# Performance work log

Hardware: AMD Instinct MI355X
Metric: run time of the kernel (lower is better)

The kernel has to match this reference:

```python
import jax, jax.numpy as jnp
import numpy as np

BATCH, SEQ, HIDDEN, HEAD, VDIM = 4, 4096, 256, 64, 64
GAMMA = 0.96875
SCALE_BASE = 512.0


def _xpos(x, downscale):
    # x: [B, L, d] ; standard RetNet XPOS (rotary + exponential position scale)
    L, d = x.shape[1], x.shape[2]
    half = d // 2
    pos = jnp.arange(L, dtype=jnp.float32)
    scale_vec = (jnp.arange(0, d, 2, dtype=jnp.float32) + 0.4 * d) / (1.4 * d)  # [d/2]
    scale = scale_vec[None, :] ** (pos[:, None] / SCALE_BASE)                   # [L, d/2]
    inv_freq = 1.0 / (10000.0 ** (jnp.arange(half, dtype=jnp.float32) / half))  # [d/2]
    sinusoid = pos[:, None] * inv_freq[None, :]                                 # [L, d/2]
    sin, cos = jnp.sin(sinusoid), jnp.cos(sinusoid)
    if downscale:
        scale = 1.0 / scale
    sin2 = jnp.repeat(sin * scale, 2, axis=-1)  # duplicate_interleave -> [L, d]
    cos2 = jnp.repeat(cos * scale, 2, axis=-1)
    x1, x2 = x[..., ::2], x[..., 1::2]
    rot = jnp.stack((-x2, x1), axis=-1).reshape(x.shape)  # rotate_every_two
    return x * cos2[None] + rot * sin2[None]


def setup_inputs() -> dict:
    key = jax.random.key(0)
    k1, k2, k3, k4 = jax.random.split(key, 4)
    X = jax.random.normal(k1, (BATCH, SEQ, HIDDEN), dtype=jnp.float32)
    W_Q = jax.random.normal(k2, (HIDDEN, HEAD), dtype=jnp.float32) / HIDDEN
    W_K = jax.random.normal(k3, (HIDDEN, HEAD), dtype=jnp.float32) / HIDDEN
    W_V = jax.random.normal(k4, (HIDDEN, VDIM), dtype=jnp.float32) / HIDDEN
    return {"X": X, "W_Q": W_Q, "W_K": W_K, "W_V": W_V}


def reference(X, W_Q, W_K, W_V):
    Q = _xpos(X @ W_Q, downscale=False)   # [B, L, d]
    K = _xpos(X @ W_K, downscale=True)    # [B, L, d]
    V = X @ W_V                           # [B, L, v]
    L = X.shape[1]
    n = jnp.arange(L)
    diff = n[:, None] - n[None, :]
    # D[n, m] = gamma^(n-m) for n >= m, else 0 (NaN/overflow-safe via clamped exponent)
    D = jnp.where(diff >= 0,
                  GAMMA ** jnp.where(diff >= 0, diff, 0).astype(jnp.float32),
                  0.0)
    scores = jnp.einsum('bnd,bmd->bnm', Q, K) * D[None]  # [B, L, L]
    return scores @ V                                     # [B, L, v]
```

## Files before the change

### kernel.cpp

```cpp
#include <hip/hip_runtime.h>
#include <hip/hip_bf16.h>
#include <math.h>


#define SEQ    4096
#define NB     4
#define HID    256
#define HD     64
#define WT     4

typedef short          bf16x8 __attribute__((ext_vector_type(8)));
typedef float          f32x4  __attribute__((ext_vector_type(4)));
typedef unsigned short u16;
typedef unsigned int   u32;
typedef u16            u16x8  __attribute__((ext_vector_type(8)));
typedef u16            u16x4  __attribute__((ext_vector_type(4)));

__device__ __forceinline__ u16 f2bf(float f) {
    __hip_bfloat16 h = __float2bfloat16(f);
    return __builtin_bit_cast(u16, h);
}

__global__ __launch_bounds__(256)
void prep_kernel(const float* __restrict__ WQ, const float* __restrict__ WK,
                 const float* __restrict__ WV, float* __restrict__ Tbl,
                 u16* __restrict__ Wf)
{
    const int t = threadIdx.x;
    if (blockIdx.x < 512) {
        const int p = blockIdx.x * 256 + t;
        const int n = p >> 5, i = p & 31;
        const float sv = (2.f * (float)i + 25.6f) / 89.6f;
        const float sc = powf(sv, (float)n * (1.f / 512.f));
        const float inv_freq = 1.f / powf(10000.f, (float)i * (1.f / 32.f));
        float sn, cs;
        sincosf((float)n * inv_freq, &sn, &cs);
        float4 o;
        o.x = cs * sc; o.y = sn * sc;
        o.z = cs / sc; o.w = sn / sc;
        reinterpret_cast<float4*>(Tbl)[p] = o;
    } else {
        const int p = (blockIdx.x - 512) * 256 + t;
        const int lane = p & 63;
        const int kc   = (p >> 6) & 7;
        const int ct   = p >> 9;
        const int col  = ct * 16 + (lane & 15);
        const float* Wsrc = (col < 64) ? WQ : (col < 128) ? WK : WV;
        const int c = col & 63;
        u16x8 hv;
#pragma unroll
        for (int j = 0; j < 8; ++j)
            hv[j] = f2bf(Wsrc[(kc * 32 + (lane >> 4) * 8 + j) * HD + c]);
        *reinterpret_cast<u16x8*>(&Wf[(size_t)p * 8]) = hv;
    }
}

#define XLDS 264

__global__ __launch_bounds__(1024, 4)
void proj_kernel(const float* __restrict__ X, const float* __restrict__ Tbl,
                 const u16* __restrict__ Wf,
                 u16* __restrict__ Qb, u16* __restrict__ Kb, u16* __restrict__ Vb)
{
    __shared__ __align__(16) u16 Xhs[64 * XLDS];
    const int t = threadIdx.x;
    const int row0 = blockIdx.x * 64;

    for (int e = t; e < 64 * 64; e += 1024) {
        const int r = e >> 6, k4 = (e & 63) << 2;
        const float4 xv = *reinterpret_cast<const float4*>(&X[(size_t)(row0 + r) * HID + k4]);
        u16x4 hv;
#pragma unroll
        for (int j = 0; j < 4; ++j) hv[j] = f2bf((&xv.x)[j]);
        *reinterpret_cast<u16x4*>(&Xhs[r * XLDS + k4]) = hv;
    }
    __syncthreads();

    const int lane = t & 63;
    const int w    = t >> 6;
    const int rt   = w >> 2;
    const int ch   = w & 3;
    const int frow = rt * 16 + (lane & 15);
    const int fk   = (lane >> 4) * 8;

    f32x4 acc[3];
#pragma unroll
    for (int i = 0; i < 3; ++i) acc[i] = (f32x4)0.f;

#pragma unroll
    for (int kc = 0; kc < 8; ++kc) {
        const bf16x8 ah = *reinterpret_cast<const bf16x8*>(&Xhs[frow * XLDS + kc * 32 + fk]);
#pragma unroll
        for (int ctp = 0; ctp < 3; ++ctp) {
            const int ct = ch * 3 + ctp;
            const size_t fb = (size_t)((ct * 8 + kc) * 64 + lane) * 8;
            const bf16x8 wh = *reinterpret_cast<const bf16x8*>(&Wf[fb]);
            acc[ctp] = __builtin_amdgcn_mfma_f32_16x16x32_bf16(ah, wh, acc[ctp], 0, 0, 0);
        }
    }

    const int sel   = lane & 1;
    const int c16   = lane & 15;
    const int rbase = (lane >> 4) * 4;

#pragma unroll
    for (int ctp = 0; ctp < 3; ++ctp) {
        const int ct = ch * 3 + ctp;
        float xp[4];
#pragma unroll
        for (int reg = 0; reg < 4; ++reg)
            xp[reg] = __shfl_xor(acc[ctp][reg], 1, 64);
#pragma unroll
        for (int rr = 0; rr < 2; ++rr) {
            const int reg = sel * 2 + rr;
            const float xe = sel ? xp[reg] : acc[ctp][reg];
            const float xo = sel ? acc[ctp][reg] : xp[reg];
            const int r = row0 + rt * 16 + rbase + reg;
            if (ct < 8) {
                const bool isK = ct >= 4;
                const int cq0 = (ct & 3) * 16 + (c16 & ~1);
                const int i   = cq0 >> 1;
                const int n   = r & (SEQ - 1);
                const float4 tb = reinterpret_cast<const float4*>(Tbl)[n * 32 + i];
                const float cs = isK ? tb.z : tb.x;
                const float sn = isK ? tb.w : tb.y;
                const float oe = xe * cs - xo * sn;
                const float oo = xo * cs + xe * sn;
                const u32 hw = (u32)f2bf(oe) | ((u32)f2bf(oo) << 16);
                u32* P = reinterpret_cast<u32*>(isK ? Kb : Qb);
                P[(r * HD + cq0) >> 1] = hw;
            } else {
                const int cv0 = (ct - 8) * 16 + (c16 & ~1);
                const u32 w32 = (u32)f2bf(xe) | ((u32)f2bf(xo) << 16);
                reinterpret_cast<u32*>(Vb)[(r * HD + cv0) >> 1] = w32;
            }
        }
    }
}

#define KRS 72
#define SW  72

__global__ __launch_bounds__(1024, 4)
void retention_kernel(const u16* __restrict__ Qb, const u16* __restrict__ Kb,
                      const u16* __restrict__ Vb, float* __restrict__ Out)
{
    __shared__ __align__(16) u16 Khs[2][64 * KRS];
    __shared__ __align__(16) u16 Vts[3][64 * KRS];
    __shared__ __align__(16) u16 Ss [2][64 * SW];

    const int t    = threadIdx.x;
    const int lane = t & 63;
    const int w    = t >> 6;
    const int rb   = w >> 2;
    const int cb   = w & 3;

    const int flat = blockIdx.x + 64 * blockIdx.y;
    const int work = (flat & 7) * 32 + (flat >> 3);
    const int nt   = work & 63;
    const int b    = work >> 6;
    const int n0   = nt * 64;
    const int bbase = b * SEQ;

    const int half = t >> 9;
    const int th   = t & 511;
    const int srow = th >> 3;
    const int scol = (th & 7) * 8;
    const int vch  = ((srow >> 3) ^ (th & 7)) & 7;
    const int vidx = vch * 8 + (srow & 7);

    const int mt0 = (nt >= WT) ? (nt - WT) : 0;

    {
        const int gk = (bbase + mt0 * 64 + srow) * HD + scol;
        if (half == 0) {
            *reinterpret_cast<u16x8*>(&Khs[0][srow * KRS + scol]) =
                *reinterpret_cast<const u16x8*>(&Kb[gk]);
        } else {
            const u16x8 vv = *reinterpret_cast<const u16x8*>(&Vb[gk]);
#pragma unroll
            for (int j = 0; j < 8; ++j)
                Vts[0][(scol + j) * KRS + vidx] = vv[j];
        }
    }

    const int frow = rb * 16 + (lane & 15);
    const int fk   = (lane >> 4) * 8;
    const size_t gq = (size_t)(bbase + n0 + frow) * HD + fk;
    const bf16x8 qb0 = *reinterpret_cast<const bf16x8*>(&Qb[gq]);
    const bf16x8 qb1 = *reinterpret_cast<const bf16x8*>(&Qb[gq + 32]);
    __syncthreads();

    const float log2g = -0.04580368544f;
    const int nlocB = rb * 16 + (lane >> 4) * 4;
    const int mloc  = cb * 16 + (lane & 15);
    float gd[4]; int dd[4];
#pragma unroll
    for (int reg = 0; reg < 4; ++reg) {
        dd[reg] = nlocB + reg - mloc;
        gd[reg] = exp2f((float)dd[reg] * log2g);
    }

    f32x4 accO = (f32x4)0.f;
    const int mrow = cb * 16 + (lane & 15);
    const int c0 = ((lane >> 4)     ^ (mrow >> 3)) & 7;
    const int c1 = (((lane >> 4) + 4) ^ (mrow >> 3)) & 7;

    int curV = 0;
    for (int mt = mt0, i = 0; mt <= nt; ++mt, ++i) {
        const int cur  = i & 1;
        const int m0   = mt * 64;
        const bool pref = (mt < nt);
        const int wV   = (curV == 2) ? 0 : curV + 1;

        u16x8 pk, pv;
        if (pref) {
            const int gk = (bbase + m0 + 64 + srow) * HD + scol;
            if (half == 0) pk = *reinterpret_cast<const u16x8*>(&Kb[gk]);
            else           pv = *reinterpret_cast<const u16x8*>(&Vb[gk]);
        }

        const bf16x8 kb0 = *reinterpret_cast<const bf16x8*>(&Khs[cur][mrow * KRS + fk]);
        const bf16x8 kb1 = *reinterpret_cast<const bf16x8*>(&Khs[cur][mrow * KRS + 32 + fk]);
        f32x4 accS = (f32x4)0.f;
        accS = __builtin_amdgcn_mfma_f32_16x16x32_bf16(qb0, kb0, accS, 0, 0, 0);
        accS = __builtin_amdgcn_mfma_f32_16x16x32_bf16(qb1, kb1, accS, 0, 0, 0);

        const float gs = exp2f((float)(n0 - m0) * log2g);
#pragma unroll
        for (int reg = 0; reg < 4; ++reg) {
            const int d   = (n0 - m0) + dd[reg];
            const float g = (d >= 0) ? gs * gd[reg] : 0.f;
            Ss[cur][(nlocB + reg) * SW + mloc] = f2bf(accS[reg] * g);
        }

        if (pref) {
            if (half == 0) {
                *reinterpret_cast<u16x8*>(&Khs[cur ^ 1][srow * KRS + scol]) = pk;
            } else {
#pragma unroll
                for (int j = 0; j < 8; ++j)
                    Vts[wV][(scol + j) * KRS + vidx] = pv[j];
            }
        }

        __syncthreads();

        const bf16x8 s0 = *reinterpret_cast<const bf16x8*>(&Ss[cur][frow * SW + fk]);
        const bf16x8 s1 = *reinterpret_cast<const bf16x8*>(&Ss[cur][frow * SW + 32 + fk]);
        const bf16x8 v0 = *reinterpret_cast<const bf16x8*>(&Vts[curV][mrow * KRS + c0 * 8]);
        const bf16x8 v1 = *reinterpret_cast<const bf16x8*>(&Vts[curV][mrow * KRS + c1 * 8]);
        accO = __builtin_amdgcn_mfma_f32_16x16x32_bf16(s0, v0, accO, 0, 0, 0);
        accO = __builtin_amdgcn_mfma_f32_16x16x32_bf16(s1, v1, accO, 0, 0, 0);

        curV = wV;
    }

    const int v = cb * 16 + (lane & 15);
#pragma unroll
    for (int reg = 0; reg < 4; ++reg) {
        const int n = n0 + rb * 16 + (lane >> 4) * 4 + reg;
        Out[(size_t)(bbase + n) * HD + v] = accO[reg];
    }
}

extern "C" void kernel_launch(void* const* d_in, const int* in_sizes, int n_in,
                              void* d_out, int out_size, void* d_ws, size_t ws_size,
                              hipStream_t stream)
{
    const float* X  = (const float*)d_in[0];
    const float* WQ = (const float*)d_in[1];
    const float* WK = (const float*)d_in[2];
    const float* WV = (const float*)d_in[3];
    float* Out = (float*)d_out;

    char* ws = (char*)d_ws;
    const size_t SZ = (size_t)NB * SEQ * HD * sizeof(u16);
    u16* Qb = (u16*)(ws);
    u16* Kb = (u16*)(ws + SZ);
    u16* Vb = (u16*)(ws + 2 * SZ);
    float* Tbl = (float*)(ws + 3 * SZ);
    u16* Wf = (u16*)(ws + 4 * SZ);

    prep_kernel<<<dim3(536), 256, 0, stream>>>(WQ, WK, WV, Tbl, Wf);
    proj_kernel<<<dim3(256), 1024, 0, stream>>>(
        X, Tbl, Wf, Qb, Kb, Vb);
    retention_kernel<<<dim3(64, NB), 1024, 0, stream>>>(
        Qb, Kb, Vb, Out);
}
```

Before: 28.46 us.

## Fuse projection and retention kernels via cooperative launch with grid sync

Merges the projection and retention kernels into one cooperative kernel. A grid-wide sync separates the two phases, and a single shared-memory buffer is reused for both. The goal is to remove one kernel launch and the gap between the two kernels. In exchange it adds the cost of a grid barrier and requires all 256 blocks to be resident at once. It also moves the Wf workspace offset.

```diff
diff --git a/kernel.cpp b/kernel.cpp
--- a/kernel.cpp
+++ b/kernel.cpp
@@ -1,4 +1,5 @@
 #include <hip/hip_runtime.h>
+#include <hip/hip_cooperative_groups.h>
 #include <hip/hip_bf16.h>
 #include <math.h>
 
@@ -8,6 +9,8 @@
 #define HID    256
 #define HD     64
 #define WT     4
+
+namespace cg = cooperative_groups;
 
 typedef short          bf16x8 __attribute__((ext_vector_type(8)));
 typedef float          f32x4  __attribute__((ext_vector_type(4)));
@@ -56,211 +59,213 @@
 }
 
 #define XLDS 264
+#define KRS  72
+#define SW   72
+#define TILE (64 * KRS)
 
 __global__ __launch_bounds__(1024, 4)
-void proj_kernel(const float* __restrict__ X, const float* __restrict__ Tbl,
-                 const u16* __restrict__ Wf,
-                 u16* __restrict__ Qb, u16* __restrict__ Kb, u16* __restrict__ Vb)
+void fused_kernel(const float* __restrict__ X, const float* __restrict__ Tbl,
+                  const u16* __restrict__ Wf,
+                  u16* __restrict__ Qb, u16* __restrict__ Kb, u16* __restrict__ Vb,
+                  float* __restrict__ Out)
 {
-    __shared__ __align__(16) u16 Xhs[64 * XLDS];
-    const int t = threadIdx.x;
-    const int row0 = blockIdx.x * 64;
-
-    for (int e = t; e < 64 * 64; e += 1024) {
-        const int r = e >> 6, k4 = (e & 63) << 2;
-        const float4 xv = *reinterpret_cast<const float4*>(&X[(size_t)(row0 + r) * HID + k4]);
-        u16x4 hv;
-#pragma unroll
-        for (int j = 0; j < 4; ++j) hv[j] = f2bf((&xv.x)[j]);
-        *reinterpret_cast<u16x4*>(&Xhs[r * XLDS + k4]) = hv;
-    }
-    __syncthreads();
-
-    const int lane = t & 63;
-    const int w    = t >> 6;
-    const int rt   = w >> 2;
-    const int ch   = w & 3;
-    const int frow = rt * 16 + (lane & 15);
-    const int fk   = (lane >> 4) * 8;
-
-    f32x4 acc[3];
-#pragma unroll
-    for (int i = 0; i < 3; ++i) acc[i] = (f32x4)0.f;
-
-#pragma unroll
-    for (int kc = 0; kc < 8; ++kc) {
-        const bf16x8 ah = *reinterpret_cast<const bf16x8*>(&Xhs[frow * XLDS + kc * 32 + fk]);
-#pragma unroll
-        for (int ctp = 0; ctp < 3; ++ctp) {
-            const int ct = ch * 3 + ctp;
-            const size_t fb = (size_t)((ct * 8 + kc) * 64 + lane) * 8;
-            const bf16x8 wh = *reinterpret_cast<const bf16x8*>(&Wf[fb]);
-            acc[ctp] = __builtin_amdgcn_mfma_f32_16x16x32_bf16(ah, wh, acc[ctp], 0, 0, 0);
-        }
-    }
-
-    const int sel   = lane & 1;
-    const int c16   = lane & 15;
-    const int rbase = (lane >> 4) * 4;
-
-#pragma unroll
-    for (int ctp = 0; ctp < 3; ++ctp) {
-        const int ct = ch * 3 + ctp;
-        float xp[4];
-#pragma unroll
-        for (int reg = 0; reg < 4; ++reg)
-            xp[reg] = __shfl_xor(acc[ctp][reg], 1, 64);
-#pragma unroll
-        for (int rr = 0; rr < 2; ++rr) {
-            const int reg = sel * 2 + rr;
-            const float xe = sel ? xp[reg] : acc[ctp][reg];
-            const float xo = sel ? acc[ctp][reg] : xp[reg];
-            const int r = row0 + rt * 16 + rbase + reg;
-            if (ct < 8) {
-                const bool isK = ct >= 4;
-                const int cq0 = (ct & 3) * 16 + (c16 & ~1);
-                const int i   = cq0 >> 1;
-                const int n   = r & (SEQ - 1);
-                const float4 tb = reinterpret_cast<const float4*>(Tbl)[n * 32 + i];
-                const float cs = isK ? tb.z : tb.x;
-                const float sn = isK ? tb.w : tb.y;
-                const float oe = xe * cs - xo * sn;
-                const float oo = xo * cs + xe * sn;
-                const u32 hw = (u32)f2bf(oe) | ((u32)f2bf(oo) << 16);
-                u32* P = reinterpret_cast<u32*>(isK ? Kb : Qb);
-                P[(r * HD + cq0) >> 1] = hw;
-            } else {
-                const int cv0 = (ct - 8) * 16 + (c16 & ~1);
-                const u32 w32 = (u32)f2bf(xe) | ((u32)f2bf(xo) << 16);
-                reinterpret_cast<u32*>(Vb)[(r * HD + cv0) >> 1] = w32;
-            }
-        }
-    }
-}
-
-#define KRS 72
-#define SW  72
-
-__global__ __launch_bounds__(1024, 4)
-void retention_kernel(const u16* __restrict__ Qb, const u16* __restrict__ Kb,
-                      const u16* __restrict__ Vb, float* __restrict__ Out)
-{
-    __shared__ __align__(16) u16 Khs[2][64 * KRS];
-    __shared__ __align__(16) u16 Vts[3][64 * KRS];
-    __shared__ __align__(16) u16 Ss [2][64 * SW];
+    __shared__ __align__(16) u16 SMEM[7 * TILE];
 
     const int t    = threadIdx.x;
     const int lane = t & 63;
     const int w    = t >> 6;
-    const int rb   = w >> 2;
-    const int cb   = w & 3;
-
-    const int flat = blockIdx.x + 64 * blockIdx.y;
-    const int work = (flat & 7) * 32 + (flat >> 3);
-    const int nt   = work & 63;
-    const int b    = work >> 6;
-    const int n0   = nt * 64;
-    const int bbase = b * SEQ;
-
-    const int half = t >> 9;
-    const int th   = t & 511;
-    const int srow = th >> 3;
-    const int scol = (th & 7) * 8;
-    const int vch  = ((srow >> 3) ^ (th & 7)) & 7;
-    const int vidx = vch * 8 + (srow & 7);
-
-    const int mt0 = (nt >= WT) ? (nt - WT) : 0;
 
     {
-        const int gk = (bbase + mt0 * 64 + srow) * HD + scol;
-        if (half == 0) {
-            *reinterpret_cast<u16x8*>(&Khs[0][srow * KRS + scol]) =
-                *reinterpret_cast<const u16x8*>(&Kb[gk]);
-        } else {
-            const u16x8 vv = *reinterpret_cast<const u16x8*>(&Vb[gk]);
-#pragma unroll
-            for (int j = 0; j < 8; ++j)
-                Vts[0][(scol + j) * KRS + vidx] = vv[j];
+        u16* Xhs = SMEM;
+        const int row0 = blockIdx.x * 64;
+
+        for (int e = t; e < 64 * 64; e += 1024) {
+            const int r = e >> 6, k4 = (e & 63) << 2;
+            const float4 xv = *reinterpret_cast<const float4*>(&X[(size_t)(row0 + r) * HID + k4]);
+            u16x4 hv;
+#pragma unroll
+            for (int j = 0; j < 4; ++j) hv[j] = f2bf((&xv.x)[j]);
+            *reinterpret_cast<u16x4*>(&Xhs[r * XLDS + k4]) = hv;
+        }
+        __syncthreads();
+
+        const int rt   = w >> 2;
+        const int ch   = w & 3;
+        const int frow = rt * 16 + (lane & 15);
+        const int fk   = (lane >> 4) * 8;
+
+        f32x4 acc[3];
+#pragma unroll
+        for (int i = 0; i < 3; ++i) acc[i] = (f32x4)0.f;
+
+#pragma unroll
+        for (int kc = 0; kc < 8; ++kc) {
+            const bf16x8 ah = *reinterpret_cast<const bf16x8*>(&Xhs[frow * XLDS + kc * 32 + fk]);
+#pragma unroll
+            for (int ctp = 0; ctp < 3; ++ctp) {
+                const int ct = ch * 3 + ctp;
+                const size_t fb = (size_t)((ct * 8 + kc) * 64 + lane) * 8;
+                const bf16x8 wh = *reinterpret_cast<const bf16x8*>(&Wf[fb]);
+                acc[ctp] = __builtin_amdgcn_mfma_f32_16x16x32_bf16(ah, wh, acc[ctp], 0, 0, 0);
+            }
+        }
+
+        const int sel   = lane & 1;
+        const int c16   = lane & 15;
+        const int rbase = (lane >> 4) * 4;
+
+#pragma unroll
+        for (int ctp = 0; ctp < 3; ++ctp) {
+            const int ct = ch * 3 + ctp;
+            float xp[4];
+#pragma unroll
+            for (int reg = 0; reg < 4; ++reg)
+                xp[reg] = __shfl_xor(acc[ctp][reg], 1, 64);
+#pragma unroll
+            for (int rr = 0; rr < 2; ++rr) {
+                const int reg = sel * 2 + rr;
+                const float xe = sel ? xp[reg] : acc[ctp][reg];
+                const float xo = sel ? acc[ctp][reg] : xp[reg];
+                const int r = row0 + rt * 16 + rbase + reg;
+                if (ct < 8) {
+                    const bool isK = ct >= 4;
+                    const int cq0 = (ct & 3) * 16 + (c16 & ~1);
+                    const int i   = cq0 >> 1;
+                    const int n   = r & (SEQ - 1);
+                    const float4 tb = reinterpret_cast<const float4*>(Tbl)[n * 32 + i];
+                    const float cs = isK ? tb.z : tb.x;
+                    const float sn = isK ? tb.w : tb.y;
+                    const float oe = xe * cs - xo * sn;
+                    const float oo = xo * cs + xe * sn;
+                    const u32 hw = (u32)f2bf(oe) | ((u32)f2bf(oo) << 16);
+                    u32* P = reinterpret_cast<u32*>(isK ? Kb : Qb);
+                    P[(r * HD + cq0) >> 1] = hw;
+                } else {
+                    const int cv0 = (ct - 8) * 16 + (c16 & ~1);
+                    const u32 w32 = (u32)f2bf(xe) | ((u32)f2bf(xo) << 16);
+                    reinterpret_cast<u32*>(Vb)[(r * HD + cv0) >> 1] = w32;
+                }
+            }
         }
     }
 
-    const int frow = rb * 16 + (lane & 15);
-    const int fk   = (lane >> 4) * 8;
-    const size_t gq = (size_t)(bbase + n0 + frow) * HD + fk;
-    const bf16x8 qb0 = *reinterpret_cast<const bf16x8*>(&Qb[gq]);
-    const bf16x8 qb1 = *reinterpret_cast<const bf16x8*>(&Qb[gq + 32]);
-    __syncthreads();
-
-    const float log2g = -0.04580368544f;
-    const int nlocB = rb * 16 + (lane >> 4) * 4;
-    const int mloc  = cb * 16 + (lane & 15);
-    float gd[4]; int dd[4];
-#pragma unroll
-    for (int reg = 0; reg < 4; ++reg) {
-        dd[reg] = nlocB + reg - mloc;
-        gd[reg] = exp2f((float)dd[reg] * log2g);
-    }
-
-    f32x4 accO = (f32x4)0.f;
-    const int mrow = cb * 16 + (lane & 15);
-    const int c0 = ((lane >> 4)     ^ (mrow >> 3)) & 7;
-    const int c1 = (((lane >> 4) + 4) ^ (mrow >> 3)) & 7;
-
-    int curV = 0;
-    for (int mt = mt0, i = 0; mt <= nt; ++mt, ++i) {
-        const int cur  = i & 1;
-        const int m0   = mt * 64;
-        const bool pref = (mt < nt);
-        const int wV   = (curV == 2) ? 0 : curV + 1;
-
-        u16x8 pk, pv;
-        if (pref) {
-            const int gk = (bbase + m0 + 64 + srow) * HD + scol;
-            if (half == 0) pk = *reinterpret_cast<const u16x8*>(&Kb[gk]);
-            else           pv = *reinterpret_cast<const u16x8*>(&Vb[gk]);
-        }
-
-        const bf16x8 kb0 = *reinterpret_cast<const bf16x8*>(&Khs[cur][mrow * KRS + fk]);
-        const bf16x8 kb1 = *reinterpret_cast<const bf16x8*>(&Khs[cur][mrow * KRS + 32 + fk]);
-        f32x4 accS = (f32x4)0.f;
-        accS = __builtin_amdgcn_mfma_f32_16x16x32_bf16(qb0, kb0, accS, 0, 0, 0);
-        accS = __builtin_amdgcn_mfma_f32_16x16x32_bf16(qb1, kb1, accS, 0, 0, 0);
-
-        const float gs = exp2f((float)(n0 - m0) * log2g);
+    cg::this_grid().sync();
+
+    {
+        u16* const KhsB = SMEM;
+        u16* const VtsB = SMEM + 2 * TILE;
+        u16* const SsB  = SMEM + 5 * TILE;
+
+        const int rb   = w >> 2;
+        const int cb   = w & 3;
+
+        const int flat = blockIdx.x;
+        const int work = (flat & 7) * 32 + (flat >> 3);
+        const int nt   = work & 63;
+        const int b    = work >> 6;
+        const int n0   = nt * 64;
+        const int bbase = b * SEQ;
+
+        const int half = t >> 9;
+        const int th   = t & 511;
+        const int srow = th >> 3;
+        const int scol = (th & 7) * 8;
+        const int vch  = ((srow >> 3) ^ (th & 7)) & 7;
+        const int vidx = vch * 8 + (srow & 7);
+
+        const int mt0 = (nt >= WT) ? (nt - WT) : 0;
+
+        {
+            const int gk = (bbase + mt0 * 64 + srow) * HD + scol;
+            if (half == 0) {
+                *reinterpret_cast<u16x8*>(&KhsB[srow * KRS + scol]) =
+                    *reinterpret_cast<const u16x8*>(&Kb[gk]);
+            } else {
+                const u16x8 vv = *reinterpret_cast<const u16x8*>(&Vb[gk]);
+#pragma unroll
+                for (int j = 0; j < 8; ++j)
+                    VtsB[(scol + j) * KRS + vidx] = vv[j];
+            }
+        }
+
+        const int frow = rb * 16 + (lane & 15);
+        const int fk   = (lane >> 4) * 8;
+        const size_t gq = (size_t)(bbase + n0 + frow) * HD + fk;
+        const bf16x8 qb0 = *reinterpret_cast<const bf16x8*>(&Qb[gq]);
+        const bf16x8 qb1 = *reinterpret_cast<const bf16x8*>(&Qb[gq + 32]);
+        __syncthreads();
+
+        const float log2g = -0.04580368544f;
+        const int nlocB = rb * 16 + (lane >> 4) * 4;
+        const int mloc  = cb * 16 + (lane & 15);
+        float gd[4]; int dd[4];
 #pragma unroll
         for (int reg = 0; reg < 4; ++reg) {
-            const int d   = (n0 - m0) + dd[reg];
-            const float g = (d >= 0) ? gs * gd[reg] : 0.f;
-            Ss[cur][(nlocB + reg) * SW + mloc] = f2bf(accS[reg] * g);
-        }
-
-        if (pref) {
-            if (half == 0) {
-                *reinterpret_cast<u16x8*>(&Khs[cur ^ 1][srow * KRS + scol]) = pk;
-            } else {
-#pragma unroll
-                for (int j = 0; j < 8; ++j)
-                    Vts[wV][(scol + j) * KRS + vidx] = pv[j];
-            }
-        }
-
-        __syncthreads();
-
-        const bf16x8 s0 = *reinterpret_cast<const bf16x8*>(&Ss[cur][frow * SW + fk]);
-        const bf16x8 s1 = *reinterpret_cast<const bf16x8*>(&Ss[cur][frow * SW + 32 + fk]);
-        const bf16x8 v0 = *reinterpret_cast<const bf16x8*>(&Vts[curV][mrow * KRS + c0 * 8]);
-        const bf16x8 v1 = *reinterpret_cast<const bf16x8*>(&Vts[curV][mrow * KRS + c1 * 8]);
-        accO = __builtin_amdgcn_mfma_f32_16x16x32_bf16(s0, v0, accO, 0, 0, 0);
-        accO = __builtin_amdgcn_mfma_f32_16x16x32_bf16(s1, v1, accO, 0, 0, 0);
-
-        curV = wV;
-    }
-
-    const int v = cb * 16 + (lane & 15);
-#pragma unroll
-    for (int reg = 0; reg < 4; ++reg) {
-        const int n = n0 + rb * 16 + (lane >> 4) * 4 + reg;
-        Out[(size_t)(bbase + n) * HD + v] = accO[reg];
+            dd[reg] = nlocB + reg - mloc;
+            gd[reg] = exp2f((float)dd[reg] * log2g);
+        }
+
+        f32x4 accO = (f32x4)0.f;
+        const int mrow = cb * 16 + (lane & 15);
+        const int c0 = ((lane >> 4)     ^ (mrow >> 3)) & 7;
+        const int c1 = (((lane >> 4) + 4) ^ (mrow >> 3)) & 7;
+
+        int curV = 0;
+        for (int mt = mt0, i = 0; mt <= nt; ++mt, ++i) {
+            const int cur  = i & 1;
+            const int m0   = mt * 64;
+            const bool pref = (mt < nt);
+            const int wV   = (curV == 2) ? 0 : curV + 1;
+
+            u16x8 pk, pv;
+            if (pref) {
+                const int gk = (bbase + m0 + 64 + srow) * HD + scol;
+                if (half == 0) pk = *reinterpret_cast<const u16x8*>(&Kb[gk]);
+                else           pv = *reinterpret_cast<const u16x8*>(&Vb[gk]);
+            }
+
+            const bf16x8 kb0 = *reinterpret_cast<const bf16x8*>(&KhsB[cur * TILE + mrow * KRS + fk]);
+            const bf16x8 kb1 = *reinterpret_cast<const bf16x8*>(&KhsB[cur * TILE + mrow * KRS + 32 + fk]);
+            f32x4 accS = (f32x4)0.f;
+            accS = __builtin_amdgcn_mfma_f32_16x16x32_bf16(qb0, kb0, accS, 0, 0, 0);
+            accS = __builtin_amdgcn_mfma_f32_16x16x32_bf16(qb1, kb1, accS, 0, 0, 0);
+
+            const float gs = exp2f((float)(n0 - m0) * log2g);
+#pragma unroll
+            for (int reg = 0; reg < 4; ++reg) {
+                const int d   = (n0 - m0) + dd[reg];
+                const float g = (d >= 0) ? gs * gd[reg] : 0.f;
+                SsB[cur * TILE + (nlocB + reg) * SW + mloc] = f2bf(accS[reg] * g);
+            }
+
+            if (pref) {
+                if (half == 0) {
+                    *reinterpret_cast<u16x8*>(&KhsB[(cur ^ 1) * TILE + srow * KRS + scol]) = pk;
+                } else {
+#pragma unroll
+                    for (int j = 0; j < 8; ++j)
+                        VtsB[wV * TILE + (scol + j) * KRS + vidx] = pv[j];
+                }
+            }
+
+            __syncthreads();
+
+            const bf16x8 s0 = *reinterpret_cast<const bf16x8*>(&SsB[cur * TILE + frow * SW + fk]);
+            const bf16x8 s1 = *reinterpret_cast<const bf16x8*>(&SsB[cur * TILE + frow * SW + 32 + fk]);
+            const bf16x8 v0 = *reinterpret_cast<const bf16x8*>(&VtsB[curV * TILE + mrow * KRS + c0 * 8]);
+            const bf16x8 v1 = *reinterpret_cast<const bf16x8*>(&VtsB[curV * TILE + mrow * KRS + c1 * 8]);
+            accO = __builtin_amdgcn_mfma_f32_16x16x32_bf16(s0, v0, accO, 0, 0, 0);
+            accO = __builtin_amdgcn_mfma_f32_16x16x32_bf16(s1, v1, accO, 0, 0, 0);
+
+            curV = wV;
+        }
+
+        const int v = cb * 16 + (lane & 15);
+#pragma unroll
+        for (int reg = 0; reg < 4; ++reg) {
+            const int n = n0 + rb * 16 + (lane >> 4) * 4 + reg;
+            Out[(size_t)(bbase + n) * HD + v] = accO[reg];
+        }
     }
 }
 
@@ -280,11 +285,13 @@
     u16* Kb = (u16*)(ws + SZ);
     u16* Vb = (u16*)(ws + 2 * SZ);
     float* Tbl = (float*)(ws + 3 * SZ);
-    u16* Wf = (u16*)(ws + 4 * SZ);
+    u16* Wf = (u16*)(ws + 3 * SZ + (2 << 20));
 
     prep_kernel<<<dim3(536), 256, 0, stream>>>(WQ, WK, WV, Tbl, Wf);
-    proj_kernel<<<dim3(256), 1024, 0, stream>>>(
-        X, Tbl, Wf, Qb, Kb, Vb);
-    retention_kernel<<<dim3(64, NB), 1024, 0, stream>>>(
-        Qb, Kb, Vb, Out);
-}
+
+    const float* Xa = X; const float* Ta = Tbl; const u16* Wa = Wf;
+    u16* Qa = Qb; u16* Ka = Kb; u16* Va = Vb; float* Oa = Out;
+    void* args[] = {&Xa, &Ta, &Wa, &Qa, &Ka, &Va, &Oa};
+    hipLaunchCooperativeKernel((const void*)fused_kernel, dim3(256), dim3(1024),
+                               args, 0, stream);
+}
```

Result: slower. 61.05 us (+114.5%).
